# Kernel tuning notes

Hardware: AMD Instinct MI355X
Metric: run time of the kernel (lower is better)

## Reference

```python
import jax, jax.numpy as jnp
import numpy as np

B, N, C = 16, 1024, 1152
H = 16
D = C // H  # 72
INNER = 4608
EPS = 1e-6


def _layernorm(x, g, b):
    mu = jnp.mean(x, axis=-1, keepdims=True)
    var = jnp.mean(jnp.square(x - mu), axis=-1, keepdims=True)
    return (x - mu) * jax.lax.rsqrt(var + EPS) * g + b


def setup_inputs() -> dict:
    key = jax.random.key(0)
    ks = jax.random.split(key, 16)
    s_c = 1.0 / np.sqrt(C)
    s_i = 1.0 / np.sqrt(INNER)
    return {
        "x": jax.random.normal(ks[0], (B, N, C), dtype=jnp.float32),
        "ln1_g": jnp.ones((C,), jnp.float32),
        "ln1_b": jnp.zeros((C,), jnp.float32),
        # weights stored (in, out) so y = x @ W + b (equiv to torch x @ W.T + b)
        "qkv_w": jax.random.normal(ks[1], (C, 3 * C), jnp.float32) * s_c,
        "qkv_b": jnp.zeros((3 * C,), jnp.float32),
        "proj_w": jax.random.normal(ks[2], (C, C), jnp.float32) * s_c,
        "proj_b": jnp.zeros((C,), jnp.float32),
        "ln2_g": jnp.ones((C,), jnp.float32),
        "ln2_b": jnp.zeros((C,), jnp.float32),
        "fc1_w": jax.random.normal(ks[3], (C, INNER), jnp.float32) * s_c,
        "fc1_b": jnp.zeros((INNER,), jnp.float32),
        "fc2_w": jax.random.normal(ks[4], (INNER, C), jnp.float32) * s_i,
        "fc2_b": jnp.zeros((C,), jnp.float32),
    }


def reference(x, ln1_g, ln1_b, qkv_w, qkv_b, proj_w, proj_b,
              ln2_g, ln2_b, fc1_w, fc1_b, fc2_w, fc2_b):
    scale = D ** -0.5
    # --- attention branch ---
    h = _layernorm(x, ln1_g, ln1_b)
    qkv = (h @ qkv_w + qkv_b).reshape(B, N, 3, H, D)
    q, k, v = jnp.moveaxis(qkv, 2, 0)            # each (B, N, H, D)
    q = q.transpose(0, 2, 1, 3)                   # (B, H, N, D)
    k = k.transpose(0, 2, 1, 3)
    v = v.transpose(0, 2, 1, 3)
    attn = jnp.einsum('bhnd,bhmd->bhnm', q, k) * scale
    attn = jax.nn.softmax(attn, axis=-1)
    out = jnp.einsum('bhnm,bhmd->bhnd', attn, v)
    out = out.transpose(0, 2, 1, 3).reshape(B, N, C)
    x = x + out @ proj_w + proj_b
    # --- MLP branch ---
    h = _layernorm(x, ln2_g, ln2_b)
    h = jax.nn.gelu(h @ fc1_w + fc1_b, approximate=False)
    x = x + h @ fc2_w + fc2_b
    return x
```

## Files before the change

kernel.cpp:

```cpp
#include <hip/hip_runtime.h>
#include <hip/hip_bf16.h>

typedef unsigned short ushort_t;
using short8 = __attribute__((ext_vector_type(8))) short;
using f32x4  = __attribute__((ext_vector_type(4))) float;

#define DEVI __device__ __forceinline__

DEVI ushort_t f2bf(float f) {
    union { float f; unsigned u; } c; c.f = f;
    unsigned u = c.u;
    return (ushort_t)((u + 0x7FFF + ((u >> 16) & 1)) >> 16);
}

DEVI f32x4 mfma16(short8 a, short8 b, f32x4 c) {
    return __builtin_amdgcn_mfma_f32_16x16x32_bf16(a, b, c, 0, 0, 0);
}

DEVI void gld16(const void* g, void* l) {
    __builtin_amdgcn_global_load_lds(
        (const __attribute__((address_space(1))) unsigned int*)g,
        (__attribute__((address_space(3))) unsigned int*)l, 16, 0, 0);
}

#define Bsz 16
#define Ntok 1024
#define Cdim 1152
#define Hn 16
#define Dh 72
#define Dp 96
#define INNER 4608
#define Mrows (Bsz * Ntok)

#define OFF_QKV_WT  ((size_t)0)
#define OFF_PROJ_WT ((size_t)7962624)
#define OFF_FC1_WT  ((size_t)10616832)
#define OFF_FC2_WT  ((size_t)21233664)
#define OFF_H       ((size_t)31850496)
#define OFF_ATT     ((size_t)69599232)
#define OFF_Q       ((size_t)107347968)
#define OFF_K       ((size_t)157679616)
#define OFF_VT      ((size_t)208011264)
#define OFF_HIDDEN  OFF_Q

__global__ __launch_bounds__(256) void transpose_cast(
    const float* __restrict__ W, ushort_t* __restrict__ Wt, int K, int N)
{
    __shared__ float t[64][65];
    const int n0 = blockIdx.x * 64;
    const int k0 = blockIdx.y * 64;
    #pragma unroll
    for (int j = 0; j < 4; ++j) {
        int idx = threadIdx.x + j * 256;
        int r = idx >> 4;
        int c4 = idx & 15;
        float4 v = *(const float4*)&W[(size_t)(k0 + r) * N + n0 + c4 * 4];
        t[r][c4 * 4 + 0] = v.x; t[r][c4 * 4 + 1] = v.y;
        t[r][c4 * 4 + 2] = v.z; t[r][c4 * 4 + 3] = v.w;
    }
    __syncthreads();
    #pragma unroll
    for (int j = 0; j < 4; ++j) {
        int idx = threadIdx.x + j * 256;
        int rn = idx >> 4;
        int c4 = idx & 15;
        ushort4 o;
        o.x = f2bf(t[c4 * 4 + 0][rn]);
        o.y = f2bf(t[c4 * 4 + 1][rn]);
        o.z = f2bf(t[c4 * 4 + 2][rn]);
        o.w = f2bf(t[c4 * 4 + 3][rn]);
        *(ushort4*)&Wt[(size_t)(n0 + rn) * K + k0 + c4 * 4] = o;
    }
}

__global__ __launch_bounds__(256) void ln_kernel(
    const float* __restrict__ x, const float* __restrict__ g,
    const float* __restrict__ b, ushort_t* __restrict__ out)
{
    const int row = blockIdx.x;
    const int tid = threadIdx.x;
    const int lane = tid & 63, wid = tid >> 6;
    const float* xr = x + (size_t)row * Cdim;

    float4 v0 = ((const float4*)xr)[tid];
    float4 v1 = {0, 0, 0, 0};
    if (tid < 32) v1 = ((const float4*)xr)[256 + tid];
    float s  = v0.x + v0.y + v0.z + v0.w + v1.x + v1.y + v1.z + v1.w;
    float s2 = v0.x*v0.x + v0.y*v0.y + v0.z*v0.z + v0.w*v0.w
             + v1.x*v1.x + v1.y*v1.y + v1.z*v1.z + v1.w*v1.w;
    #pragma unroll
    for (int off = 32; off >= 1; off >>= 1) {
        s  += __shfl_xor(s, off);
        s2 += __shfl_xor(s2, off);
    }
    __shared__ float red[8];
    if (lane == 0) { red[wid] = s; red[4 + wid] = s2; }
    __syncthreads();
    s  = red[0] + red[1] + red[2] + red[3];
    s2 = red[4] + red[5] + red[6] + red[7];
    const float mu = s * (1.0f / Cdim);
    const float var = s2 * (1.0f / Cdim) - mu * mu;
    const float rs = rsqrtf(var + 1e-6f);

    ushort_t* orow = out + (size_t)row * Cdim;
    {
        float4 g4 = ((const float4*)g)[tid];
        float4 b4 = ((const float4*)b)[tid];
        ushort4 o;
        o.x = f2bf((v0.x - mu) * rs * g4.x + b4.x);
        o.y = f2bf((v0.y - mu) * rs * g4.y + b4.y);
        o.z = f2bf((v0.z - mu) * rs * g4.z + b4.z);
        o.w = f2bf((v0.w - mu) * rs * g4.w + b4.w);
        ((ushort4*)orow)[tid] = o;
    }
    if (tid < 32) {
        float4 g4 = ((const float4*)g)[256 + tid];
        float4 b4 = ((const float4*)b)[256 + tid];
        ushort4 o;
        o.x = f2bf((v1.x - mu) * rs * g4.x + b4.x);
        o.y = f2bf((v1.y - mu) * rs * g4.y + b4.y);
        o.z = f2bf((v1.z - mu) * rs * g4.z + b4.z);
        o.w = f2bf((v1.w - mu) * rs * g4.w + b4.w);
        ((ushort4*)orow)[256 + tid] = o;
    }
}

enum { EPI_QKV = 0, EPI_PROJ = 1, EPI_FC1 = 2, EPI_FC2 = 3 };

#define TBM 256
#define TBN 128
#define TBK 64
#define BUFB 49152

template<int EPI, int N, int K>
__global__ __launch_bounds__(512, 2) void gemm_bt(
    const ushort_t* __restrict__ A, const ushort_t* __restrict__ Bt,
    const float* __restrict__ bias, const float* __restrict__ resid,
    float* __restrict__ outf, ushort_t* __restrict__ outb,
    ushort_t* __restrict__ outq, ushort_t* __restrict__ outk, ushort_t* __restrict__ outv)
{
    __shared__ ushort_t smem[3 * BUFB / 2];
    const int tid = threadIdx.x;
    const int lane = tid & 63, wid = tid >> 6;
    const int wr = wid >> 1, wc = wid & 1;
    const int fr = lane & 15, fq = lane >> 4;
    const int m0 = blockIdx.y * TBM;
    const int n0 = blockIdx.x * TBN;

    const ushort_t* Ag = A + (size_t)m0 * K;
    const ushort_t* Bg = Bt + (size_t)n0 * K;

    size_t srcA[4]; int dstA[4];
    #pragma unroll
    for (int r = 0; r < 4; ++r) {
        const int chunk = r * 512 + tid;
        const int row = chunk >> 3;
        const int slot = chunk & 7;
        srcA[r] = (size_t)row * K + (slot ^ (row & 7)) * 8;
        dstA[r] = (r * 512 + wid * 64) * 16;
    }
    size_t srcB[2]; int dstB[2];
    #pragma unroll
    for (int r = 0; r < 2; ++r) {
        const int chunk = r * 512 + tid;
        const int row = chunk >> 3;
        const int slot = chunk & 7;
        srcB[r] = (size_t)row * K + (slot ^ (row & 7)) * 8;
        dstB[r] = 32768 + (r * 512 + wid * 64) * 16;
    }

    auto STAGE = [&](int buf, int kk) {
        char* lb = (char*)smem + (size_t)buf * BUFB;
        #pragma unroll
        for (int r = 0; r < 4; ++r) gld16(Ag + srcA[r] + kk, lb + dstA[r]);
        #pragma unroll
        for (int r = 0; r < 2; ++r) gld16(Bg + srcB[r] + kk, lb + dstB[r]);
    };

    const int swz = (fr & 7) << 4;
    int aoff[4][2], boff[4][2];
    #pragma unroll
    for (int i = 0; i < 4; ++i)
        #pragma unroll
        for (int kh = 0; kh < 2; ++kh) {
            const int rowA = wr * 64 + i * 16 + fr;
            aoff[i][kh] = rowA * 128 + ((kh * 64 + fq * 16) ^ swz);
            const int rowB = wc * 64 + i * 16 + fr;
            boff[i][kh] = 32768 + rowB * 128 + ((kh * 64 + fq * 16) ^ swz);
        }

    f32x4 acc[4][4] = {};
    const int NT = K / TBK;

    STAGE(0, 0);
    STAGE(1, TBK);

    auto COMPUTE = [&](int t) {
        const char* lb = (const char*)smem + (size_t)(t % 3) * BUFB;
        #pragma unroll
        for (int kh = 0; kh < 2; ++kh) {
            short8 a[4], b[4];
            #pragma unroll
            for (int i = 0; i < 4; ++i) {
                a[i] = *(const short8*)(lb + aoff[i][kh]);
                b[i] = *(const short8*)(lb + boff[i][kh]);
            }
            __builtin_amdgcn_s_setprio(1);
            #pragma unroll
            for (int mi = 0; mi < 4; ++mi)
                #pragma unroll
                for (int ni = 0; ni < 4; ++ni)
                    acc[mi][ni] = mfma16(a[mi], b[ni], acc[mi][ni]);
            __builtin_amdgcn_s_setprio(0);
        }
    };

    for (int t = 0; t < NT - 1; ++t) {
        asm volatile("s_waitcnt vmcnt(6)" ::: "memory");
        __builtin_amdgcn_s_barrier();
        __builtin_amdgcn_sched_barrier(0);
        if (t + 2 < NT) STAGE((t + 2) % 3, (t + 2) * TBK);
        __builtin_amdgcn_sched_barrier(0);
        COMPUTE(t);
    }
    asm volatile("s_waitcnt vmcnt(0)" ::: "memory");
    __builtin_amdgcn_s_barrier();
    __builtin_amdgcn_sched_barrier(0);
    COMPUTE(NT - 1);

    #pragma unroll
    for (int mi = 0; mi < 4; ++mi) {
        #pragma unroll
        for (int ni = 0; ni < 4; ++ni) {
            const int col = n0 + wc * 64 + ni * 16 + fr;
            const int rbase = m0 + wr * 64 + mi * 16 + fq * 4;
            #pragma unroll
            for (int i = 0; i < 4; ++i) {
                const int r = rbase + i;
                float v = acc[mi][ni][i];
                if (EPI == EPI_QKV) {
                    v += bias[col];
                    const int which = col / Cdim;
                    const int rc = col % Cdim;
                    const int h = rc / Dh, d = rc % Dh;
                    const int b = r >> 10, n = r & 1023;
                    const size_t head = (size_t)(b * Hn + h);
                    if (which == 0)      outq[(head * Ntok + n) * Dp + d] = f2bf(v);
                    else if (which == 1) outk[(head * Ntok + n) * Dp + d] = f2bf(v);
                    else                 outv[(head * Dp + d) * Ntok + n] = f2bf(v);
                } else if (EPI == EPI_PROJ) {
                    v += bias[col] + resid[(size_t)r * N + col];
                    outf[(size_t)r * N + col] = v;
                } else if (EPI == EPI_FC1) {
                    v += bias[col];
                    v = 0.5f * v * (1.0f + erff(v * 0.70710678118f));
                    outb[(size_t)r * N + col] = f2bf(v);
                } else {
                    v += bias[col] + outf[(size_t)r * N + col];
                    outf[(size_t)r * N + col] = v;
                }
            }
        }
    }
}

__global__ __launch_bounds__(256) void attn_kernel(
    const ushort_t* __restrict__ q, const ushort_t* __restrict__ k,
    const ushort_t* __restrict__ vt, ushort_t* __restrict__ out)
{
    const int tid = threadIdx.x;
    const int lane = tid & 63, wid = tid >> 6;
    const int bh = blockIdx.y;
    const int qbase = blockIdx.x * 128 + wid * 32;
    const int fr = lane & 15, fq = lane >> 4;
    const ushort_t* qh = q  + (size_t)bh * Ntok * Dp;
    const ushort_t* kh = k  + (size_t)bh * Ntok * Dp;
    const ushort_t* vh = vt + (size_t)bh * Dp * Ntok;

    short8 aq[2][3];
    #pragma unroll
    for (int t = 0; t < 2; ++t)
        #pragma unroll
        for (int ks = 0; ks < 3; ++ks)
            aq[t][ks] = *(const short8*)&qh[(size_t)(qbase + t * 16 + fr) * Dp + ks * 32 + fq * 8];

    f32x4 o[2][5] = {};
    float mrun[2][4], lsum[2][4];
    #pragma unroll
    for (int t = 0; t < 2; ++t)
        #pragma unroll
        for (int i = 0; i < 4; ++i) { mrun[t][i] = -1e30f; lsum[t][i] = 0.0f; }

    __shared__ ushort_t plds[4][2][16][32];
    const float scale = 0.117851130f;

    for (int kv = 0; kv < Ntok; kv += 32) {
        short8 kb0[3], kb1[3], bv[5];
        #pragma unroll
        for (int ks = 0; ks < 3; ++ks) {
            kb0[ks] = *(const short8*)&kh[(size_t)(kv + fr) * Dp + ks * 32 + fq * 8];
            kb1[ks] = *(const short8*)&kh[(size_t)(kv + 16 + fr) * Dp + ks * 32 + fq * 8];
        }
        #pragma unroll
        for (int dt = 0; dt < 5; ++dt)
            bv[dt] = *(const short8*)&vh[(size_t)(dt * 16 + fr) * Ntok + kv + fq * 8];

        f32x4 s[2][2] = {};
        __builtin_amdgcn_s_setprio(1);
        #pragma unroll
        for (int ks = 0; ks < 3; ++ks)
            #pragma unroll
            for (int t = 0; t < 2; ++t) {
                s[t][0] = mfma16(aq[t][ks], kb0[ks], s[t][0]);
                s[t][1] = mfma16(aq[t][ks], kb1[ks], s[t][1]);
            }
        __builtin_amdgcn_s_setprio(0);

        #pragma unroll
        for (int t = 0; t < 2; ++t) {
            float a0[4], a1[4];
            float lmax = -1e30f;
            #pragma unroll
            for (int i = 0; i < 4; ++i) {
                a0[i] = s[t][0][i] * scale;
                a1[i] = s[t][1][i] * scale;
                lmax = fmaxf(lmax, fmaxf(a0[i], a1[i]));
            }
            const float mmin = fminf(fminf(mrun[t][0], mrun[t][1]),
                                     fminf(mrun[t][2], mrun[t][3]));
            if (!__all(lmax <= mmin + 8.0f)) {
                #pragma unroll
                for (int i = 0; i < 4; ++i) {
                    float mx = fmaxf(a0[i], a1[i]);
                    mx = fmaxf(mx, __shfl_xor(mx, 1));
                    mx = fmaxf(mx, __shfl_xor(mx, 2));
                    mx = fmaxf(mx, __shfl_xor(mx, 4));
                    mx = fmaxf(mx, __shfl_xor(mx, 8));
                    const float mnew = fmaxf(mrun[t][i], mx);
                    const float f = __expf(mrun[t][i] - mnew);
                    mrun[t][i] = mnew;
                    lsum[t][i] *= f;
                    #pragma unroll
                    for (int dt = 0; dt < 5; ++dt) o[t][dt][i] *= f;
                }
            }
            #pragma unroll
            for (int i = 0; i < 4; ++i) {
                float p0 = __expf(a0[i] - mrun[t][i]);
                float p1 = __expf(a1[i] - mrun[t][i]);
                lsum[t][i] += p0 + p1;
                plds[wid][t][fq * 4 + i][fr]      = f2bf(p0);
                plds[wid][t][fq * 4 + i][16 + fr] = f2bf(p1);
            }
        }
        short8 pa[2];
        #pragma unroll
        for (int t = 0; t < 2; ++t)
            pa[t] = *(const short8*)&plds[wid][t][fr][fq * 8];
        __builtin_amdgcn_s_setprio(1);
        #pragma unroll
        for (int dt = 0; dt < 5; ++dt)
            #pragma unroll
            for (int t = 0; t < 2; ++t)
                o[t][dt] = mfma16(pa[t], bv[dt], o[t][dt]);
        __builtin_amdgcn_s_setprio(0);
    }

    const int b = bh >> 4, h = bh & 15;
    #pragma unroll
    for (int t = 0; t < 2; ++t) {
        float inv[4];
        #pragma unroll
        for (int i = 0; i < 4; ++i) {
            float s = lsum[t][i];
            s += __shfl_xor(s, 1);
            s += __shfl_xor(s, 2);
            s += __shfl_xor(s, 4);
            s += __shfl_xor(s, 8);
            inv[i] = 1.0f / s;
        }
        #pragma unroll
        for (int dt = 0; dt < 5; ++dt) {
            const int d = dt * 16 + fr;
            if (d < Dh) {
                #pragma unroll
                for (int i = 0; i < 4; ++i) {
                    const size_t idx = ((size_t)(b * Ntok) + qbase + t * 16 + fq * 4 + i) * Cdim + h * Dh + d;
                    out[idx] = f2bf(o[t][dt][i] * inv[i]);
                }
            }
        }
    }
}

extern "C" void kernel_launch(void* const* d_in, const int* in_sizes, int n_in,
                              void* d_out, int out_size, void* d_ws, size_t ws_size,
                              hipStream_t stream) {
    const float* x      = (const float*)d_in[0];
    const float* ln1_g  = (const float*)d_in[1];
    const float* ln1_b  = (const float*)d_in[2];
    const float* qkv_w  = (const float*)d_in[3];
    const float* qkv_b  = (const float*)d_in[4];
    const float* proj_w = (const float*)d_in[5];
    const float* proj_b = (const float*)d_in[6];
    const float* ln2_g  = (const float*)d_in[7];
    const float* ln2_b  = (const float*)d_in[8];
    const float* fc1_w  = (const float*)d_in[9];
    const float* fc1_b  = (const float*)d_in[10];
    const float* fc2_w  = (const float*)d_in[11];
    const float* fc2_b  = (const float*)d_in[12];

    char* ws = (char*)d_ws;
    ushort_t* qkv_wT  = (ushort_t*)(ws + OFF_QKV_WT);
    ushort_t* proj_wT = (ushort_t*)(ws + OFF_PROJ_WT);
    ushort_t* fc1_wT  = (ushort_t*)(ws + OFF_FC1_WT);
    ushort_t* fc2_wT  = (ushort_t*)(ws + OFF_FC2_WT);
    ushort_t* hbuf    = (ushort_t*)(ws + OFF_H);
    ushort_t* attnout = (ushort_t*)(ws + OFF_ATT);
    ushort_t* qb      = (ushort_t*)(ws + OFF_Q);
    ushort_t* kb      = (ushort_t*)(ws + OFF_K);
    ushort_t* vtb     = (ushort_t*)(ws + OFF_VT);
    ushort_t* hidden  = (ushort_t*)(ws + OFF_HIDDEN);
    float* out = (float*)d_out;

    hipMemsetAsync(ws + OFF_Q, 0, (size_t)3 * 50331648, stream);

    transpose_cast<<<dim3(3 * Cdim / 64, Cdim / 64), 256, 0, stream>>>(qkv_w, qkv_wT, Cdim, 3 * Cdim);
    transpose_cast<<<dim3(Cdim / 64, Cdim / 64), 256, 0, stream>>>(proj_w, proj_wT, Cdim, Cdim);
    transpose_cast<<<dim3(INNER / 64, Cdim / 64), 256, 0, stream>>>(fc1_w, fc1_wT, Cdim, INNER);
    transpose_cast<<<dim3(Cdim / 64, INNER / 64), 256, 0, stream>>>(fc2_w, fc2_wT, INNER, Cdim);

    ln_kernel<<<Mrows, 256, 0, stream>>>(x, ln1_g, ln1_b, hbuf);

    gemm_bt<EPI_QKV, 3 * Cdim, Cdim><<<dim3(27, Mrows / TBM), 512, 0, stream>>>(
        hbuf, qkv_wT, qkv_b, nullptr, nullptr, nullptr, qb, kb, vtb);

    attn_kernel<<<dim3(Ntok / 128, Bsz * Hn), 256, 0, stream>>>(qb, kb, vtb, attnout);

    gemm_bt<EPI_PROJ, Cdim, Cdim><<<dim3(9, Mrows / TBM), 512, 0, stream>>>(
        attnout, proj_wT, proj_b, x, out, nullptr, nullptr, nullptr, nullptr);

    ln_kernel<<<Mrows, 256, 0, stream>>>(out, ln2_g, ln2_b, hbuf);

    gemm_bt<EPI_FC1, INNER, Cdim><<<dim3(36, Mrows / TBM), 512, 0, stream>>>(
        hbuf, fc1_wT, fc1_b, nullptr, nullptr, hidden, nullptr, nullptr, nullptr);

    gemm_bt<EPI_FC2, Cdim, INNER><<<dim3(9, Mrows / TBM), 512, 0, stream>>>(
        hidden, fc2_wT, fc2_b, nullptr, out, nullptr, nullptr, nullptr, nullptr);
}
```

Measured before the change: 1.133 ms.

## Enlarge GEMM tile to 256x256 with double-buffered LDS pipeline

The GEMM block tile grows from 256x128 to 256x256, with each of the 8 waves computing a 128x64 sub-tile, which raises operand reuse per LDS load. LDS buffering drops from triple to double buffering (2x64KB) to fit the larger tile. The grids now round up, so weight buffers are padded and column guards are added in the epilogue. The cost is more accumulator registers per thread, lower occupancy, shallower prefetch, and padded tiles that waste compute when N=1152 or 3456 is not a multiple of 256.

```diff
diff --git a/kernel.cpp b/kernel.cpp
--- a/kernel.cpp
+++ b/kernel.cpp
@@ -33,14 +33,14 @@
 #define Mrows (Bsz * Ntok)
 
 #define OFF_QKV_WT  ((size_t)0)
-#define OFF_PROJ_WT ((size_t)7962624)
-#define OFF_FC1_WT  ((size_t)10616832)
-#define OFF_FC2_WT  ((size_t)21233664)
-#define OFF_H       ((size_t)31850496)
-#define OFF_ATT     ((size_t)69599232)
-#define OFF_Q       ((size_t)107347968)
-#define OFF_K       ((size_t)157679616)
-#define OFF_VT      ((size_t)208011264)
+#define OFF_PROJ_WT ((size_t)8257536)
+#define OFF_FC1_WT  ((size_t)11206656)
+#define OFF_FC2_WT  ((size_t)21823488)
+#define OFF_H       ((size_t)33619968)
+#define OFF_ATT     ((size_t)71368704)
+#define OFF_Q       ((size_t)109117440)
+#define OFF_K       ((size_t)159449088)
+#define OFF_VT      ((size_t)209780736)
 #define OFF_HIDDEN  OFF_Q
 
 __global__ __launch_bounds__(256) void transpose_cast(
@@ -128,9 +128,9 @@
 enum { EPI_QKV = 0, EPI_PROJ = 1, EPI_FC1 = 2, EPI_FC2 = 3 };
 
 #define TBM 256
-#define TBN 128
+#define TBN 256
 #define TBK 64
-#define BUFB 49152
+#define BUFB 65536
 
 template<int EPI, int N, int K>
 __global__ __launch_bounds__(512, 2) void gemm_bt(
@@ -139,10 +139,10 @@
     float* __restrict__ outf, ushort_t* __restrict__ outb,
     ushort_t* __restrict__ outq, ushort_t* __restrict__ outk, ushort_t* __restrict__ outv)
 {
-    __shared__ ushort_t smem[3 * BUFB / 2];
+    __shared__ ushort_t smem[2 * BUFB / 2];
     const int tid = threadIdx.x;
     const int lane = tid & 63, wid = tid >> 6;
-    const int wr = wid >> 1, wc = wid & 1;
+    const int wr = wid >> 2, wc = wid & 3;
     const int fr = lane & 15, fq = lane >> 4;
     const int m0 = blockIdx.y * TBM;
     const int n0 = blockIdx.x * TBN;
@@ -150,23 +150,16 @@
     const ushort_t* Ag = A + (size_t)m0 * K;
     const ushort_t* Bg = Bt + (size_t)n0 * K;
 
-    size_t srcA[4]; int dstA[4];
+    size_t srcA[4], srcB[4]; int dstA[4], dstB[4];
     #pragma unroll
     for (int r = 0; r < 4; ++r) {
         const int chunk = r * 512 + tid;
         const int row = chunk >> 3;
         const int slot = chunk & 7;
         srcA[r] = (size_t)row * K + (slot ^ (row & 7)) * 8;
+        srcB[r] = srcA[r];
         dstA[r] = (r * 512 + wid * 64) * 16;
-    }
-    size_t srcB[2]; int dstB[2];
-    #pragma unroll
-    for (int r = 0; r < 2; ++r) {
-        const int chunk = r * 512 + tid;
-        const int row = chunk >> 3;
-        const int slot = chunk & 7;
-        srcB[r] = (size_t)row * K + (slot ^ (row & 7)) * 8;
-        dstB[r] = 32768 + (r * 512 + wid * 64) * 16;
+        dstB[r] = 32768 + dstA[r];
     }
 
     auto STAGE = [&](int buf, int kk) {
@@ -174,40 +167,37 @@
         #pragma unroll
         for (int r = 0; r < 4; ++r) gld16(Ag + srcA[r] + kk, lb + dstA[r]);
         #pragma unroll
-        for (int r = 0; r < 2; ++r) gld16(Bg + srcB[r] + kk, lb + dstB[r]);
+        for (int r = 0; r < 4; ++r) gld16(Bg + srcB[r] + kk, lb + dstB[r]);
     };
 
     const int swz = (fr & 7) << 4;
-    int aoff[4][2], boff[4][2];
-    #pragma unroll
-    for (int i = 0; i < 4; ++i)
+    int aoff[8][2], boff[4][2];
+    #pragma unroll
+    for (int kh = 0; kh < 2; ++kh) {
+        const int colb = (kh * 64 + fq * 16) ^ swz;
+        #pragma unroll
+        for (int i = 0; i < 8; ++i)
+            aoff[i][kh] = (wr * 128 + i * 16 + fr) * 128 + colb;
+        #pragma unroll
+        for (int i = 0; i < 4; ++i)
+            boff[i][kh] = 32768 + (wc * 64 + i * 16 + fr) * 128 + colb;
+    }
+
+    f32x4 acc[8][4] = {};
+    const int NT = K / TBK;
+
+    auto COMPUTE = [&](int t) {
+        const char* lb = (const char*)smem + (size_t)(t & 1) * BUFB;
         #pragma unroll
         for (int kh = 0; kh < 2; ++kh) {
-            const int rowA = wr * 64 + i * 16 + fr;
-            aoff[i][kh] = rowA * 128 + ((kh * 64 + fq * 16) ^ swz);
-            const int rowB = wc * 64 + i * 16 + fr;
-            boff[i][kh] = 32768 + rowB * 128 + ((kh * 64 + fq * 16) ^ swz);
-        }
-
-    f32x4 acc[4][4] = {};
-    const int NT = K / TBK;
-
-    STAGE(0, 0);
-    STAGE(1, TBK);
-
-    auto COMPUTE = [&](int t) {
-        const char* lb = (const char*)smem + (size_t)(t % 3) * BUFB;
-        #pragma unroll
-        for (int kh = 0; kh < 2; ++kh) {
-            short8 a[4], b[4];
-            #pragma unroll
-            for (int i = 0; i < 4; ++i) {
-                a[i] = *(const short8*)(lb + aoff[i][kh]);
-                b[i] = *(const short8*)(lb + boff[i][kh]);
-            }
+            short8 a[8], b[4];
+            #pragma unroll
+            for (int i = 0; i < 8; ++i) a[i] = *(const short8*)(lb + aoff[i][kh]);
+            #pragma unroll
+            for (int i = 0; i < 4; ++i) b[i] = *(const short8*)(lb + boff[i][kh]);
             __builtin_amdgcn_s_setprio(1);
             #pragma unroll
-            for (int mi = 0; mi < 4; ++mi)
+            for (int mi = 0; mi < 8; ++mi)
                 #pragma unroll
                 for (int ni = 0; ni < 4; ++ni)
                     acc[mi][ni] = mfma16(a[mi], b[ni], acc[mi][ni]);
@@ -215,49 +205,52 @@
         }
     };
 
-    for (int t = 0; t < NT - 1; ++t) {
-        asm volatile("s_waitcnt vmcnt(6)" ::: "memory");
+    STAGE(0, 0);
+    for (int t = 0; t < NT; ++t) {
+        if (t + 1 < NT) {
+            STAGE((t + 1) & 1, (t + 1) * TBK);
+            asm volatile("s_waitcnt vmcnt(8)" ::: "memory");
+        } else {
+            asm volatile("s_waitcnt vmcnt(0)" ::: "memory");
+        }
         __builtin_amdgcn_s_barrier();
         __builtin_amdgcn_sched_barrier(0);
-        if (t + 2 < NT) STAGE((t + 2) % 3, (t + 2) * TBK);
-        __builtin_amdgcn_sched_barrier(0);
         COMPUTE(t);
-    }
-    asm volatile("s_waitcnt vmcnt(0)" ::: "memory");
-    __builtin_amdgcn_s_barrier();
-    __builtin_amdgcn_sched_barrier(0);
-    COMPUTE(NT - 1);
-
-    #pragma unroll
-    for (int mi = 0; mi < 4; ++mi) {
+        if (t + 1 < NT) __builtin_amdgcn_s_barrier();
+    }
+
+    #pragma unroll
+    for (int mi = 0; mi < 8; ++mi) {
         #pragma unroll
         for (int ni = 0; ni < 4; ++ni) {
             const int col = n0 + wc * 64 + ni * 16 + fr;
-            const int rbase = m0 + wr * 64 + mi * 16 + fq * 4;
-            #pragma unroll
-            for (int i = 0; i < 4; ++i) {
-                const int r = rbase + i;
-                float v = acc[mi][ni][i];
-                if (EPI == EPI_QKV) {
-                    v += bias[col];
-                    const int which = col / Cdim;
-                    const int rc = col % Cdim;
-                    const int h = rc / Dh, d = rc % Dh;
-                    const int b = r >> 10, n = r & 1023;
-                    const size_t head = (size_t)(b * Hn + h);
-                    if (which == 0)      outq[(head * Ntok + n) * Dp + d] = f2bf(v);
-                    else if (which == 1) outk[(head * Ntok + n) * Dp + d] = f2bf(v);
-                    else                 outv[(head * Dp + d) * Ntok + n] = f2bf(v);
-                } else if (EPI == EPI_PROJ) {
-                    v += bias[col] + resid[(size_t)r * N + col];
-                    outf[(size_t)r * N + col] = v;
-                } else if (EPI == EPI_FC1) {
-                    v += bias[col];
-                    v = 0.5f * v * (1.0f + erff(v * 0.70710678118f));
-                    outb[(size_t)r * N + col] = f2bf(v);
-                } else {
-                    v += bias[col] + outf[(size_t)r * N + col];
-                    outf[(size_t)r * N + col] = v;
+            if (col < N) {
+                const int rbase = m0 + wr * 128 + mi * 16 + fq * 4;
+                #pragma unroll
+                for (int i = 0; i < 4; ++i) {
+                    const int r = rbase + i;
+                    float v = acc[mi][ni][i];
+                    if (EPI == EPI_QKV) {
+                        v += bias[col];
+                        const int which = col / Cdim;
+                        const int rc = col % Cdim;
+                        const int h = rc / Dh, d = rc % Dh;
+                        const int b = r >> 10, n = r & 1023;
+                        const size_t head = (size_t)(b * Hn + h);
+                        if (which == 0)      outq[(head * Ntok + n) * Dp + d] = f2bf(v);
+                        else if (which == 1) outk[(head * Ntok + n) * Dp + d] = f2bf(v);
+                        else                 outv[(head * Dp + d) * Ntok + n] = f2bf(v);
+                    } else if (EPI == EPI_PROJ) {
+                        v += bias[col] + resid[(size_t)r * N + col];
+                        outf[(size_t)r * N + col] = v;
+                    } else if (EPI == EPI_FC1) {
+                        v += bias[col];
+                        v = 0.5f * v * (1.0f + erff(v * 0.70710678118f));
+                        outb[(size_t)r * N + col] = f2bf(v);
+                    } else {
+                        v += bias[col] + outf[(size_t)r * N + col];
+                        outf[(size_t)r * N + col] = v;
+                    }
                 }
             }
         }
@@ -432,19 +425,19 @@
 
     ln_kernel<<<Mrows, 256, 0, stream>>>(x, ln1_g, ln1_b, hbuf);
 
-    gemm_bt<EPI_QKV, 3 * Cdim, Cdim><<<dim3(27, Mrows / TBM), 512, 0, stream>>>(
+    gemm_bt<EPI_QKV, 3 * Cdim, Cdim><<<dim3(14, Mrows / TBM), 512, 0, stream>>>(
         hbuf, qkv_wT, qkv_b, nullptr, nullptr, nullptr, qb, kb, vtb);
 
     attn_kernel<<<dim3(Ntok / 128, Bsz * Hn), 256, 0, stream>>>(qb, kb, vtb, attnout);
 
-    gemm_bt<EPI_PROJ, Cdim, Cdim><<<dim3(9, Mrows / TBM), 512, 0, stream>>>(
+    gemm_bt<EPI_PROJ, Cdim, Cdim><<<dim3(5, Mrows / TBM), 512, 0, stream>>>(
         attnout, proj_wT, proj_b, x, out, nullptr, nullptr, nullptr, nullptr);
 
     ln_kernel<<<Mrows, 256, 0, stream>>>(out, ln2_g, ln2_b, hbuf);
 
-    gemm_bt<EPI_FC1, INNER, Cdim><<<dim3(36, Mrows / TBM), 512, 0, stream>>>(
+    gemm_bt<EPI_FC1, INNER, Cdim><<<dim3(18, Mrows / TBM), 512, 0, stream>>>(
         hbuf, fc1_wT, fc1_b, nullptr, nullptr, hidden, nullptr, nullptr, nullptr);
 
-    gemm_bt<EPI_FC2, Cdim, INNER><<<dim3(9, Mrows / TBM), 512, 0, stream>>>(
+    gemm_bt<EPI_FC2, Cdim, INNER><<<dim3(5, Mrows / TBM), 512, 0, stream>>>(
         hidden, fc2_wT, fc2_b, nullptr, out, nullptr, nullptr, nullptr, nullptr);
 }
```

Result: slower. 1.221 ms (+7.8%).

## Make GEMMs persistent with cross-tile prefetch pipeline across output tiles

Applied to the files above, without the earlier changes.

Converts the bf16 GEMM kernel into a persistent kernel launched with 256 workgroups, each looping over output tiles strided by 256 with column-major tile order. The three-buffer global_load_lds pipeline continues across tile boundaries, so loads for the next tile are issued while the current tile's last k-steps and epilogue run. Launch bounds drop to one block per SIMD set, giving more registers. This aims to remove per-tile prologue/drain bubbles and tail waves, at the cost of occupancy and a fixed 256-CU assumption. Workspace offsets are also shifted.

```diff
diff --git a/kernel.cpp b/kernel.cpp
--- a/kernel.cpp
+++ b/kernel.cpp
@@ -33,14 +33,14 @@
 #define Mrows (Bsz * Ntok)
 
 #define OFF_QKV_WT  ((size_t)0)
-#define OFF_PROJ_WT ((size_t)7962624)
-#define OFF_FC1_WT  ((size_t)10616832)
-#define OFF_FC2_WT  ((size_t)21233664)
-#define OFF_H       ((size_t)31850496)
-#define OFF_ATT     ((size_t)69599232)
-#define OFF_Q       ((size_t)107347968)
-#define OFF_K       ((size_t)157679616)
-#define OFF_VT      ((size_t)208011264)
+#define OFF_PROJ_WT ((size_t)8257536)
+#define OFF_FC1_WT  ((size_t)11206656)
+#define OFF_FC2_WT  ((size_t)21823488)
+#define OFF_H       ((size_t)33619968)
+#define OFF_ATT     ((size_t)71368704)
+#define OFF_Q       ((size_t)109117440)
+#define OFF_K       ((size_t)159449088)
+#define OFF_VT      ((size_t)209780736)
 #define OFF_HIDDEN  OFF_Q
 
 __global__ __launch_bounds__(256) void transpose_cast(
@@ -133,7 +133,7 @@
 #define BUFB 49152
 
 template<int EPI, int N, int K>
-__global__ __launch_bounds__(512, 2) void gemm_bt(
+__global__ __launch_bounds__(512, 1) void gemm_bt(
     const ushort_t* __restrict__ A, const ushort_t* __restrict__ Bt,
     const float* __restrict__ bias, const float* __restrict__ resid,
     float* __restrict__ outf, ushort_t* __restrict__ outb,
@@ -144,59 +144,74 @@
     const int lane = tid & 63, wid = tid >> 6;
     const int wr = wid >> 1, wc = wid & 1;
     const int fr = lane & 15, fq = lane >> 4;
-    const int m0 = blockIdx.y * TBM;
-    const int n0 = blockIdx.x * TBN;
-
-    const ushort_t* Ag = A + (size_t)m0 * K;
-    const ushort_t* Bg = Bt + (size_t)n0 * K;
+    const int bid = blockIdx.x;
+    constexpr int NTt = K / TBK;
+    constexpr int NTN = N / TBN;
+    constexpr int TT  = (Mrows / TBM) * NTN;
 
     size_t srcA[4]; int dstA[4];
     #pragma unroll
     for (int r = 0; r < 4; ++r) {
         const int chunk = r * 512 + tid;
-        const int row = chunk >> 3;
-        const int slot = chunk & 7;
+        const int row = chunk >> 3, slot = chunk & 7;
         srcA[r] = (size_t)row * K + (slot ^ (row & 7)) * 8;
-        dstA[r] = (r * 512 + wid * 64) * 16;
+        dstA[r] = chunk * 16;
     }
     size_t srcB[2]; int dstB[2];
     #pragma unroll
     for (int r = 0; r < 2; ++r) {
         const int chunk = r * 512 + tid;
-        const int row = chunk >> 3;
-        const int slot = chunk & 7;
+        const int row = chunk >> 3, slot = chunk & 7;
         srcB[r] = (size_t)row * K + (slot ^ (row & 7)) * 8;
-        dstB[r] = 32768 + (r * 512 + wid * 64) * 16;
-    }
-
-    auto STAGE = [&](int buf, int kk) {
-        char* lb = (char*)smem + (size_t)buf * BUFB;
-        #pragma unroll
-        for (int r = 0; r < 4; ++r) gld16(Ag + srcA[r] + kk, lb + dstA[r]);
-        #pragma unroll
-        for (int r = 0; r < 2; ++r) gld16(Bg + srcB[r] + kk, lb + dstB[r]);
-    };
-
+        dstB[r] = 32768 + chunk * 16;
+    }
     const int swz = (fr & 7) << 4;
     int aoff[4][2], boff[4][2];
     #pragma unroll
-    for (int i = 0; i < 4; ++i)
-        #pragma unroll
-        for (int kh = 0; kh < 2; ++kh) {
-            const int rowA = wr * 64 + i * 16 + fr;
-            aoff[i][kh] = rowA * 128 + ((kh * 64 + fq * 16) ^ swz);
-            const int rowB = wc * 64 + i * 16 + fr;
-            boff[i][kh] = 32768 + rowB * 128 + ((kh * 64 + fq * 16) ^ swz);
-        }
+    for (int kh = 0; kh < 2; ++kh) {
+        const int colb = (kh * 64 + fq * 16) ^ swz;
+        #pragma unroll
+        for (int i = 0; i < 4; ++i) {
+            aoff[i][kh] = (wr * 64 + i * 16 + fr) * 128 + colb;
+            boff[i][kh] = 32768 + (wc * 64 + i * 16 + fr) * 128 + colb;
+        }
+    }
+
+    const int nj = (TT - bid + 255) / 256;
+    const int total_u = nj * NTt;
+
+    int js = 0, ts = 0, sbuf = 0;
+    const ushort_t *sAb, *sBb;
+    auto setbases = [&](int j) {
+        int s = bid + j * 256; if (s >= TT) s = bid;
+        const int mt = s & 63, nt = s >> 6;
+        sAb = A + (size_t)(mt * TBM) * K;
+        sBb = Bt + (size_t)(nt * TBN) * K;
+    };
+    setbases(0);
+    auto STAGE = [&]() {
+        char* lb = (char*)smem + (size_t)sbuf * BUFB;
+        const ushort_t* Ab = sAb + ts * TBK;
+        const ushort_t* Bb = sBb + ts * TBK;
+        #pragma unroll
+        for (int r = 0; r < 4; ++r) gld16(Ab + srcA[r], lb + dstA[r]);
+        #pragma unroll
+        for (int r = 0; r < 2; ++r) gld16(Bb + srcB[r], lb + dstB[r]);
+        sbuf = (sbuf == 2) ? 0 : sbuf + 1;
+        if (++ts == NTt) { ts = 0; setbases(++js); }
+    };
 
     f32x4 acc[4][4] = {};
-    const int NT = K / TBK;
-
-    STAGE(0, 0);
-    STAGE(1, TBK);
-
-    auto COMPUTE = [&](int t) {
-        const char* lb = (const char*)smem + (size_t)(t % 3) * BUFB;
+    STAGE(); STAGE();
+
+    int jc = 0, tc = 0, cbuf = 0;
+    for (int u = 0; u < total_u; ++u) {
+        asm volatile("s_waitcnt vmcnt(6)" ::: "memory");
+        __builtin_amdgcn_s_barrier();
+        __builtin_amdgcn_sched_barrier(0);
+        STAGE();
+        __builtin_amdgcn_sched_barrier(0);
+        const char* lb = (const char*)smem + (size_t)cbuf * BUFB;
         #pragma unroll
         for (int kh = 0; kh < 2; ++kh) {
             short8 a[4], b[4];
@@ -213,53 +228,48 @@
                     acc[mi][ni] = mfma16(a[mi], b[ni], acc[mi][ni]);
             __builtin_amdgcn_s_setprio(0);
         }
-    };
-
-    for (int t = 0; t < NT - 1; ++t) {
-        asm volatile("s_waitcnt vmcnt(6)" ::: "memory");
-        __builtin_amdgcn_s_barrier();
-        __builtin_amdgcn_sched_barrier(0);
-        if (t + 2 < NT) STAGE((t + 2) % 3, (t + 2) * TBK);
-        __builtin_amdgcn_sched_barrier(0);
-        COMPUTE(t);
-    }
-    asm volatile("s_waitcnt vmcnt(0)" ::: "memory");
-    __builtin_amdgcn_s_barrier();
-    __builtin_amdgcn_sched_barrier(0);
-    COMPUTE(NT - 1);
-
-    #pragma unroll
-    for (int mi = 0; mi < 4; ++mi) {
-        #pragma unroll
-        for (int ni = 0; ni < 4; ++ni) {
-            const int col = n0 + wc * 64 + ni * 16 + fr;
-            const int rbase = m0 + wr * 64 + mi * 16 + fq * 4;
-            #pragma unroll
-            for (int i = 0; i < 4; ++i) {
-                const int r = rbase + i;
-                float v = acc[mi][ni][i];
-                if (EPI == EPI_QKV) {
-                    v += bias[col];
-                    const int which = col / Cdim;
-                    const int rc = col % Cdim;
-                    const int h = rc / Dh, d = rc % Dh;
-                    const int b = r >> 10, n = r & 1023;
-                    const size_t head = (size_t)(b * Hn + h);
-                    if (which == 0)      outq[(head * Ntok + n) * Dp + d] = f2bf(v);
-                    else if (which == 1) outk[(head * Ntok + n) * Dp + d] = f2bf(v);
-                    else                 outv[(head * Dp + d) * Ntok + n] = f2bf(v);
-                } else if (EPI == EPI_PROJ) {
-                    v += bias[col] + resid[(size_t)r * N + col];
-                    outf[(size_t)r * N + col] = v;
-                } else if (EPI == EPI_FC1) {
-                    v += bias[col];
-                    v = 0.5f * v * (1.0f + erff(v * 0.70710678118f));
-                    outb[(size_t)r * N + col] = f2bf(v);
-                } else {
-                    v += bias[col] + outf[(size_t)r * N + col];
-                    outf[(size_t)r * N + col] = v;
+        cbuf = (cbuf == 2) ? 0 : cbuf + 1;
+
+        if (++tc == NTt) {
+            tc = 0;
+            const int s = bid + jc * 256;
+            const int m0 = (s & 63) * TBM, n0 = (s >> 6) * TBN;
+            #pragma unroll
+            for (int mi = 0; mi < 4; ++mi) {
+                #pragma unroll
+                for (int ni = 0; ni < 4; ++ni) {
+                    const int col = n0 + wc * 64 + ni * 16 + fr;
+                    const int rbase = m0 + wr * 64 + mi * 16 + fq * 4;
+                    #pragma unroll
+                    for (int i = 0; i < 4; ++i) {
+                        const int r = rbase + i;
+                        float v = acc[mi][ni][i];
+                        if (EPI == EPI_QKV) {
+                            v += bias[col];
+                            const int which = col / Cdim;
+                            const int rc = col % Cdim;
+                            const int h = rc / Dh, d = rc % Dh;
+                            const int b2 = r >> 10, n = r & 1023;
+                            const size_t head = (size_t)(b2 * Hn + h);
+                            if (which == 0)      outq[(head * Ntok + n) * Dp + d] = f2bf(v);
+                            else if (which == 1) outk[(head * Ntok + n) * Dp + d] = f2bf(v);
+                            else                 outv[(head * Dp + d) * Ntok + n] = f2bf(v);
+                        } else if (EPI == EPI_PROJ) {
+                            v += bias[col] + resid[(size_t)r * N + col];
+                            outf[(size_t)r * N + col] = v;
+                        } else if (EPI == EPI_FC1) {
+                            v += bias[col];
+                            v = 0.5f * v * (1.0f + erff(v * 0.70710678118f));
+                            outb[(size_t)r * N + col] = f2bf(v);
+                        } else {
+                            v += bias[col] + outf[(size_t)r * N + col];
+                            outf[(size_t)r * N + col] = v;
+                        }
+                        acc[mi][ni][i] = 0.0f;
+                    }
                 }
             }
+            ++jc;
         }
     }
 }
@@ -432,19 +442,19 @@
 
     ln_kernel<<<Mrows, 256, 0, stream>>>(x, ln1_g, ln1_b, hbuf);
 
-    gemm_bt<EPI_QKV, 3 * Cdim, Cdim><<<dim3(27, Mrows / TBM), 512, 0, stream>>>(
+    gemm_bt<EPI_QKV, 3 * Cdim, Cdim><<<256, 512, 0, stream>>>(
         hbuf, qkv_wT, qkv_b, nullptr, nullptr, nullptr, qb, kb, vtb);
 
     attn_kernel<<<dim3(Ntok / 128, Bsz * Hn), 256, 0, stream>>>(qb, kb, vtb, attnout);
 
-    gemm_bt<EPI_PROJ, Cdim, Cdim><<<dim3(9, Mrows / TBM), 512, 0, stream>>>(
+    gemm_bt<EPI_PROJ, Cdim, Cdim><<<256, 512, 0, stream>>>(
         attnout, proj_wT, proj_b, x, out, nullptr, nullptr, nullptr, nullptr);
 
     ln_kernel<<<Mrows, 256, 0, stream>>>(out, ln2_g, ln2_b, hbuf);
 
-    gemm_bt<EPI_FC1, INNER, Cdim><<<dim3(36, Mrows / TBM), 512, 0, stream>>>(
+    gemm_bt<EPI_FC1, INNER, Cdim><<<256, 512, 0, stream>>>(
         hbuf, fc1_wT, fc1_b, nullptr, nullptr, hidden, nullptr, nullptr, nullptr);
 
-    gemm_bt<EPI_FC2, Cdim, INNER><<<dim3(9, Mrows / TBM), 512, 0, stream>>>(
+    gemm_bt<EPI_FC2, Cdim, INNER><<<256, 512, 0, stream>>>(
         hidden, fc2_wT, fc2_b, nullptr, out, nullptr, nullptr, nullptr, nullptr);
 }
```

Measured after the change: 1.058 ms. 6.6% less time.
